# Optimization experiments

Measured on AMD Instinct MI355X. Metric: run time of the kernel, lower is better.

The kernel has to match this reference:

```python
import jax, jax.numpy as jnp
import numpy as np

B, L, K = 16, 512, 30          # proteins, residues per protein, kNN neighbors
N = B * L
H, FC = 32, 3                  # h_channels, frame_channels
C = H + FC                     # fused sphere channels (35)
HEADS, AC, VC = 8, 16, 8       # heads, alpha channels (H//2), value channels (H//4)
RBF_N, POS_N = 16, 16
EF = RBF_N + POS_N

# idealized backbone atom positions (N, CA, C) in the local residue frame
IDEAL_BB = np.array([[-0.525, 1.363, 0.0], [0.0, 0.0, 0.0], [1.526, 0.0, 0.0]], dtype=np.float32)
# cartesian (x,y,z) -> real-SH l=1 ordering (y,z,x)
P_SH = np.array([[0., 1., 0.], [0., 0., 1.], [1., 0., 0.]], dtype=np.float32)


def _knn_edges(trans):
    # per-chain brute-force kNN (chains are contiguous blocks of length L)
    X = trans.reshape(B, L, 3)
    d2 = jnp.sum((X[:, :, None, :] - X[:, None, :, :]) ** 2, axis=-1)  # [B,L,L]
    d2 = d2 + jnp.eye(L, dtype=d2.dtype) * 1e9                          # exclude self
    _, idx = jax.lax.top_k(-d2, K)                                      # [B,L,K]
    off = (jnp.arange(B) * L)[:, None, None]
    src = (idx + off).reshape(-1)              # neighbor (edge_index[0])
    tgt = jnp.repeat(jnp.arange(N), K)         # center   (edge_index[1])
    return src, tgt


def _edge_rot_mat(vec):
    # rotation aligning the edge vector with the y axis (eSCN init_edge_rot_mat style)
    nx = vec / (jnp.linalg.norm(vec, axis=-1, keepdims=True) + 1e-12)
    ref = jnp.where(jnp.abs(nx[:, :1]) < 0.9,
                    jnp.array([1., 0., 0.], dtype=vec.dtype),
                    jnp.array([0., 0., 1.], dtype=vec.dtype))
    nz = jnp.cross(nx, ref)
    nz = nz / (jnp.linalg.norm(nz, axis=-1, keepdims=True) + 1e-12)
    ny = jnp.cross(nx, nz)
    ny = ny / (jnp.linalg.norm(ny, axis=-1, keepdims=True) + 1e-12)
    return jnp.stack([nz, nx, ny], axis=-2)  # [E,3,3]


def _rbf(d, d_min=0.0, d_max=20.0, count=RBF_N):
    mu = jnp.linspace(d_min, d_max, count)
    sigma = (d_max - d_min) / count
    return jnp.exp(-(((d[:, None] - mu) / sigma) ** 2))


def _pos_emb(src, tgt, num=POS_N):
    d = (src - tgt).astype(jnp.float32)
    freq = jnp.exp(jnp.arange(0, num, 2, dtype=jnp.float32) * (-np.log(10000.0) / num))
    ang = d[:, None] * freq
    return jnp.concatenate([jnp.cos(ang), jnp.sin(ang)], axis=-1)


def _forward(rots, trans, node_emb, batch, x_mask, noising_mask,
             W_alpha, a_vec, W_v, W_o, W_g, W_2):
    src, tgt = _knn_edges(trans)
    vec = trans[src] - trans[tgt]
    dist = jnp.linalg.norm(vec, axis=-1)
    valid = jnp.isfinite(dist) & (dist > 1e-3)  # edge_select, applied as mask

    R = _edge_rot_mat(vec)
    P = jnp.asarray(P_SH)
    D1 = jnp.einsum('ij,ejk,lk->eil', P, R, P)  # l=1 Wigner in real-SH basis [E,3,3]

    edge_features = jnp.concatenate([_rbf(dist), _pos_emb(src, tgt)], axis=-1)  # [E,32]

    # fuse node features with backbone frame atoms and editability flag
    frame_atoms = jnp.einsum('nij,aj->nai', rots, jnp.asarray(IDEAL_BB))  # [N,3atoms,3xyz]
    editable = noising_mask & (~x_mask)
    emb = jnp.zeros((N, 4, C), dtype=node_emb.dtype)
    emb = emb.at[:, :, :H].set(node_emb)
    emb = emb.at[:, 1:4, H:].set(jnp.swapaxes(frame_atoms, -1, -2))
    emb = emb.at[:, 0, C - 1].set(editable.astype(node_emb.dtype))

    # gather + rotate source features into edge frames
    xs = emb[src]                                                   # [E,4,C]
    xs_rot = jnp.concatenate([xs[:, :1], jnp.einsum('eij,ejc->eic', D1, xs[:, 1:])], axis=1)

    # invariant attention logits (l=0 of rotated src, l=0 of tgt, edge feats)
    inv = jnp.concatenate([xs_rot[:, 0], emb[tgt, 0], edge_features], axis=-1)  # [E,102]
    hdn = jax.nn.silu(inv @ W_alpha).reshape(-1, HEADS, AC)
    logits = jax.nn.leaky_relu(jnp.einsum('ehk,hk->eh', hdn, a_vec), 0.2)
    logits = jnp.where(valid[:, None], logits, -1e9)

    # segment softmax over incoming edges of each target node
    mx = jax.lax.stop_gradient(jax.ops.segment_max(logits, tgt, num_segments=N))
    ex = jnp.exp(logits - mx[tgt]) * valid[:, None].astype(logits.dtype)
    den = jax.ops.segment_sum(ex, tgt, num_segments=N)
    alpha = ex / (den[tgt] + 1e-9)                                  # [E,HEADS]

    # equivariant values, attention-weighted, rotate back, scatter
    v = (xs_rot @ W_v).reshape(-1, 4, HEADS, VC)
    m = (v * alpha[:, None, :, None]).reshape(-1, 4, HEADS * VC)
    m = jnp.concatenate([m[:, :1], jnp.einsum('eji,ejc->eic', D1, m[:, 1:])], axis=1)  # D^T
    agg = jax.ops.segment_sum(m, tgt, num_segments=N)               # [N,4,64]

    y = agg @ W_o                                                    # [N,4,H]
    gate = jax.nn.silu(y[:, 0] @ W_g)                                # invariant gating FFN
    return (y * gate[:, None, :]) @ W_2                              # [N,4,H]


def setup_inputs():
    key = jax.random.key(0)
    ks = jax.random.split(key, 12)
    rots = jax.vmap(lambda m: jnp.linalg.qr(m)[0])(jax.random.normal(ks[0], (N, 3, 3)))
    trans = jax.random.normal(ks[1], (N, 3)) * 10.0
    node_emb = jax.random.normal(ks[2], (N, 4, H))
    batch = jnp.repeat(jnp.arange(B, dtype=jnp.int32), L)
    x_mask = jax.random.randint(ks[3], (N,), 0, 2).astype(bool)
    noising_mask = jax.random.randint(ks[4], (N,), 0, 2).astype(bool)
    s = lambda k, sh, fan: jax.random.normal(k, sh) / np.sqrt(fan)
    return dict(rots=rots, trans=trans, node_emb=node_emb, batch=batch,
                x_mask=x_mask, noising_mask=noising_mask,
                W_alpha=s(ks[5], (2 * C + EF, HEADS * AC), 2 * C + EF),
                a_vec=s(ks[6], (HEADS, AC), AC),
                W_v=s(ks[7], (C, HEADS * VC), C),
                W_o=s(ks[8], (HEADS * VC, H), HEADS * VC),
                W_g=s(ks[9], (H, H), H),
                W_2=s(ks[10], (H, H), H))


def reference(rots, trans, node_emb, batch, x_mask, noising_mask,
              W_alpha, a_vec, W_v, W_o, W_g, W_2):
    return _forward(rots, trans, node_emb, batch, x_mask, noising_mask,
                    W_alpha, a_vec, W_v, W_o, W_g, W_2)
```

## Files before the change

kernel.cpp:

```cpp
#include <hip/hip_runtime.h>
#include <cstdint>

#define B_ 16
#define L_ 512
#define N_ 8192
#define K_ 30
#define E_ (N_*K_)
#define H_ 32
#define C_ 35

typedef uint16_t u16;
typedef uint32_t u32;
typedef unsigned long long u64;
typedef float f2v __attribute__((ext_vector_type(2)));

static __device__ __forceinline__ f2v splat2(float x) { f2v v; v.x = x; v.y = x; return v; }

static __device__ __forceinline__ float ldf(const void* p, int i, int bf) {
    return bf ? __uint_as_float(((u32)((const u16*)p)[i]) << 16)
              : ((const float*)p)[i];
}
static __device__ __forceinline__ float bfu16(u16 x) {
    return __uint_as_float(((u32)x) << 16);
}
static __device__ __forceinline__ int ldmask(const void* p, int i, int mode) {
    if (mode == 0) return ((const unsigned char*)p)[i] != 0;
    if (mode == 2) return ((const u32*)p)[2*i] != 0;
    return ((const u32*)p)[i] != 0;
}
static __device__ __forceinline__ u16 f2bf(float f) {
    u32 x = __float_as_uint(f);
    u32 r = x + 0x7FFFu + ((x >> 16) & 1u);
    return (u16)(r >> 16);
}
static __device__ __forceinline__ float fsilu(float x) {
    return x * __builtin_amdgcn_rcpf(1.f + __expf(-x));
}
static __device__ __forceinline__ float RL(float x, int i) {
    return __uint_as_float((u32)__builtin_amdgcn_readlane((int)__float_as_uint(x), i));
}

static __device__ __forceinline__ int detect_bf(const void* tr, int lane) {
    const u16* p = (const u16*)tr;
    int cnt = 0;
    for (int i = lane; i < 256; i += 64) {
        u16 v = p[2 * i];
        int e = (v >> 7) & 0xFF;
        if ((e >= 100 && e <= 141) || (v & 0x7FFFu) == 0) cnt++;
    }
    #pragma unroll
    for (int d = 1; d < 64; d <<= 1) cnt += __shfl_xor(cnt, d, 64);
    return cnt >= 192;
}
static __device__ __forceinline__ int detect_mm(const void* xmv, int lane) {
    const u32* xm = (const u32*)xmv;
    int anyBig = 0, oddNZ = 0;
    for (int i = lane; i < 1024; i += 64) {
        u32 w = xm[i];
        if (w & ~1u) anyBig = 1;
        if ((i & 1) && w) oddNZ = 1;
    }
    #pragma unroll
    for (int d = 1; d < 64; d <<= 1) {
        anyBig |= __shfl_xor(anyBig, d, 64);
        oddNZ  |= __shfl_xor(oddNZ, d, 64);
    }
    return anyBig ? 0 : (oddNZ ? 1 : 2);
}

__constant__ float cBB[9] = {-0.525f, 1.363f, 0.f,  0.f, 0.f, 0.f,  1.526f, 0.f, 0.f};

#define DPP_UMIN(var, CTRL) \
    { u32 o_ = (u32)__builtin_amdgcn_update_dpp((int)(var), (int)(var), CTRL, 0xF, 0xF, false); \
      (var) = (o_ < (var)) ? o_ : (var); }
#define DPP_UMIN_ALL(var) \
    DPP_UMIN(var, 0x111) DPP_UMIN(var, 0x112) DPP_UMIN(var, 0x114) \
    DPP_UMIN(var, 0x118) DPP_UMIN(var, 0x142) DPP_UMIN(var, 0x143)

#define DPP_ADD8(part) \
    part += __uint_as_float((u32)__builtin_amdgcn_update_dpp( \
        (int)__float_as_uint(part), (int)__float_as_uint(part), 0xB1, 0xF, 0xF, false)); \
    part += __uint_as_float((u32)__builtin_amdgcn_update_dpp( \
        (int)__float_as_uint(part), (int)__float_as_uint(part), 0x4E, 0xF, 0xF, false)); \
    part += __uint_as_float((u32)__builtin_amdgcn_update_dpp( \
        (int)__float_as_uint(part), (int)__float_as_uint(part), 0x141, 0xF, 0xF, false));

__global__ __launch_bounds__(256) void knn_kernel(const void* __restrict__ trans,
                                                  const void* __restrict__ xm,
                                                  int* __restrict__ flag,
                                                  int* __restrict__ srcArr)
{
    __shared__ float sX[L_], sY[L_], sZ[L_];
    __shared__ int flagS[1];
    const int bid = blockIdx.x, tid = threadIdx.x;
    const int lane = tid & 63, wid = tid >> 6;

    if (wid == 0) {
        int bf = detect_bf(trans, lane);
        if (bid == 0) {
            int mm = detect_mm(xm, lane);
            if (lane == 0) { flag[0] = bf; flag[1] = mm; }
        }
        if (lane == 0) flagS[0] = bf;
    }
    __syncthreads();
    const int bf = flagS[0];
    const int t0 = bid * 4;
    const int base = (t0 >> 9) << 9;
    if (bf) {
        const u16* tp = (const u16*)trans;
        for (int i = tid; i < L_; i += 256) {
            sX[i] = bfu16(tp[(base + i) * 3 + 0]);
            sY[i] = bfu16(tp[(base + i) * 3 + 1]);
            sZ[i] = bfu16(tp[(base + i) * 3 + 2]);
        }
    } else {
        const float* tp = (const float*)trans;
        for (int i = tid; i < L_; i += 256) {
            sX[i] = tp[(base + i) * 3 + 0];
            sY[i] = tp[(base + i) * 3 + 1];
            sZ[i] = tp[(base + i) * 3 + 2];
        }
    }
    __syncthreads();

    const int t = t0 + wid;
    const int l = t & 511;
    const float tx = sX[l], ty = sY[l], tz = sZ[l];

    u32 d2b[8];
    #pragma unroll
    for (int i = 0; i < 8; ++i) {
        int j = lane + (i << 6);
        float dx = __fsub_rn(tx, sX[j]);
        float dy = __fsub_rn(ty, sY[j]);
        float dz = __fsub_rn(tz, sZ[j]);
        float d2 = __fadd_rn(__fadd_rn(__fmul_rn(dx, dx), __fmul_rn(dy, dy)), __fmul_rn(dz, dz));
        if (j == l) d2 = __fadd_rn(d2, 1e9f);
        d2b[i] = __float_as_uint(d2);
    }

    int myres = 0;
    for (int k = 0; k < K_; ++k) {
        u32 bb = d2b[0]; int bs = 0;
        #pragma unroll
        for (int i = 1; i < 8; ++i)
            if (d2b[i] < bb) { bb = d2b[i]; bs = i; }
        u32 m = bb;
        DPP_UMIN_ALL(m)
        u32 gbits = (u32)__builtin_amdgcn_readlane((int)m, 63);
        u64 mask = __ballot(bb == gbits);
        u32 gidx;
        if (__popcll(mask) == 1) {
            int wl = __ffsll((long long)mask) - 1;
            gidx = (u32)__builtin_amdgcn_readlane((int)((bs << 6) | lane), wl);
        } else {
            u32 cand = (bb == gbits) ? (u32)((bs << 6) | lane) : 0xFFFFFFFFu;
            DPP_UMIN_ALL(cand)
            gidx = (u32)__builtin_amdgcn_readlane((int)cand, 63);
        }
        if (lane == (u32)k) myres = (int)(gidx & 511u);
        if ((gidx & 63u) == (u32)lane) {
            int ws = (int)(gidx >> 6);
            #pragma unroll
            for (int i = 0; i < 8; ++i)
                if (ws == i) d2b[i] = 0xFFFFFFFFu;
        }
    }
    if (lane < K_) srcArr[t * K_ + lane] = base + myres;
}

__global__ __launch_bounds__(256) void prep_kernel(
    const void* __restrict__ rots, const void* __restrict__ node,
    const void* __restrict__ xm, const void* __restrict__ nm,
    const void* __restrict__ Wa, const void* __restrict__ av,
    const void* __restrict__ Wv, const void* __restrict__ Wo,
    const void* __restrict__ Wg, const void* __restrict__ W2,
    const int* __restrict__ flag,
    float* __restrict__ hsrc, float* __restrict__ htgt,
    float* __restrict__ ptab, float* __restrict__ V,
    float* __restrict__ c_wrb, float* __restrict__ c_av,
    float* __restrict__ c_Wo, float* __restrict__ c_Wg, float* __restrict__ c_W2)
{
    const int bid = blockIdx.x, tid = threadIdx.x;
    const int lane = tid & 63, wid = tid >> 6;
    const int bf = flag[0], mm = flag[1];

    if (bid < 2048) {
        const int n = bid * 4 + wid;

        float eA, eB, eC = 0.f;
        {
            int s = lane;
            int r = s / 35, c = s - r * 35;
            if (c < H_)      eA = ldf(node, n * 128 + r * 32 + c, bf);
            else if (r == 0) eA = (c == 34) ? ((ldmask(nm, n, mm) && !ldmask(xm, n, mm)) ? 1.f : 0.f) : 0.f;
            else {
                int i = r - 1, a = c - 32;
                eA = ldf(rots, n*9 + i*3 + 0, bf) * cBB[a*3 + 0]
                   + ldf(rots, n*9 + i*3 + 1, bf) * cBB[a*3 + 1]
                   + ldf(rots, n*9 + i*3 + 2, bf) * cBB[a*3 + 2];
            }
            s = lane + 64;
            r = s / 35; c = s - r * 35;
            if (c < H_)      eB = ldf(node, n * 128 + r * 32 + c, bf);
            else {
                int i = r - 1, a = c - 32;
                eB = ldf(rots, n*9 + i*3 + 0, bf) * cBB[a*3 + 0]
                   + ldf(rots, n*9 + i*3 + 1, bf) * cBB[a*3 + 1]
                   + ldf(rots, n*9 + i*3 + 2, bf) * cBB[a*3 + 2];
            }
            if (lane < 12) {
                s = lane + 128;
                r = s / 35; c = s - r * 35;
                if (c < H_)      eC = ldf(node, n * 128 + r * 32 + c, bf);
                else {
                    int i = r - 1, a = c - 32;
                    eC = ldf(rots, n*9 + i*3 + 0, bf) * cBB[a*3 + 0]
                       + ldf(rots, n*9 + i*3 + 1, bf) * cBB[a*3 + 1]
                       + ldf(rots, n*9 + i*3 + 2, bf) * cBB[a*3 + 2];
                }
            }
        }

        float a0 = 0.f, a1 = 0.f, b0 = 0.f, b1 = 0.f;
        float v0 = 0.f, v1 = 0.f, v2 = 0.f, v3 = 0.f;
        if (bf) {
            const u16* wa = (const u16*)Wa;
            const u16* wv = (const u16*)Wv;
            #pragma unroll
            for (int i = 0; i < 35; ++i) {
                float ei = RL(eA, i);
                a0 = fmaf(ei, bfu16(wa[i * 128 + lane]),        a0);
                a1 = fmaf(ei, bfu16(wa[i * 128 + lane + 64]),   a1);
                b0 = fmaf(ei, bfu16(wa[(35 + i) * 128 + lane]),      b0);
                b1 = fmaf(ei, bfu16(wa[(35 + i) * 128 + lane + 64]), b1);
            }
            #pragma unroll
            for (int cp = 0; cp < 35; ++cp) {
                float w = bfu16(wv[cp * 64 + lane]);
                float e1 = (35 + cp < 64) ? RL(eA, 35 + cp) : RL(eB, cp - 29);
                float e3 = (cp < 23) ? RL(eB, 41 + cp) : RL(eC, cp - 23);
                v0 = fmaf(RL(eA, cp), w, v0);
                v1 = fmaf(e1, w, v1);
                v2 = fmaf(RL(eB, cp + 6), w, v2);
                v3 = fmaf(e3, w, v3);
            }
        } else {
            const float* wa = (const float*)Wa;
            const float* wv = (const float*)Wv;
            #pragma unroll
            for (int i = 0; i < 35; ++i) {
                float ei = RL(eA, i);
                a0 = fmaf(ei, wa[i * 128 + lane],        a0);
                a1 = fmaf(ei, wa[i * 128 + lane + 64],   a1);
                b0 = fmaf(ei, wa[(35 + i) * 128 + lane],      b0);
                b1 = fmaf(ei, wa[(35 + i) * 128 + lane + 64], b1);
            }
            #pragma unroll
            for (int cp = 0; cp < 35; ++cp) {
                float w = wv[cp * 64 + lane];
                float e1 = (35 + cp < 64) ? RL(eA, 35 + cp) : RL(eB, cp - 29);
                float e3 = (cp < 23) ? RL(eB, 41 + cp) : RL(eC, cp - 23);
                v0 = fmaf(RL(eA, cp), w, v0);
                v1 = fmaf(e1, w, v1);
                v2 = fmaf(RL(eB, cp + 6), w, v2);
                v3 = fmaf(e3, w, v3);
            }
        }
        hsrc[(size_t)n * 128 + lane]      = a0;
        hsrc[(size_t)n * 128 + lane + 64] = a1;
        htgt[(size_t)n * 128 + lane]      = b0;
        htgt[(size_t)n * 128 + lane + 64] = b1;
        float* vp = V + (size_t)n * 256 + lane;
        vp[0] = v0; vp[64] = v1; vp[128] = v2; vp[192] = v3;

    } else if (bid < 2560) {
        const int d   = (bid - 2048) * 2 + (tid >> 7);
        const int col = tid & 127;
        float dd = (float)(d - 512);
        float acc = 0.f;
        if (bf) {
            const u16* wa = (const u16*)Wa;
            #pragma unroll
            for (int q = 0; q < 8; ++q) {
                float fr = expf((float)(2 * q) * (-0.5756462732485115f));
                float ang = dd * fr;
                acc = fmaf(cosf(ang), bfu16(wa[(86 + q) * 128 + col]), acc);
                acc = fmaf(sinf(ang), bfu16(wa[(94 + q) * 128 + col]), acc);
            }
        } else {
            const float* wa = (const float*)Wa;
            #pragma unroll
            for (int q = 0; q < 8; ++q) {
                float fr = expf((float)(2 * q) * (-0.5756462732485115f));
                float ang = dd * fr;
                acc = fmaf(cosf(ang), wa[(86 + q) * 128 + col], acc);
                acc = fmaf(sinf(ang), wa[(94 + q) * 128 + col], acc);
            }
        }
        ptab[(size_t)d * 128 + col] = acc;

    } else {
        int g0 = (bid - 2560) * 256 + tid;
        for (int i = g0; i < 6272; i += 2048) {
            if      (i < 2048) c_wrb[i]        = ldf(Wa, 70 * 128 + i, bf);
            else if (i < 2176) c_av[i - 2048]  = ldf(av, i - 2048, bf);
            else if (i < 4224) c_Wo[i - 2176]  = ldf(Wo, i - 2176, bf);
            else if (i < 5248) c_Wg[i - 4224]  = ldf(Wg, i - 4224, bf);
            else               c_W2[i - 5248]  = ldf(W2, i - 5248, bf);
        }
    }
}

__global__ __launch_bounds__(128) void logits_kernel(
    const void* __restrict__ trans, const int* __restrict__ srcArr,
    const float* __restrict__ hsrc, const float* __restrict__ htgt,
    const float* __restrict__ ptab,
    const float* __restrict__ c_wrb, const float* __restrict__ c_av,
    const int* __restrict__ flag, float* __restrict__ logitsw)
{
    __shared__ float rbfS[2][32][20];
    __shared__ int   srcS[2][32];
    __shared__ int   tgtS[2][32];
    __shared__ int   dS[2][32];
    __shared__ float lgS[2][256];
    const int tid = threadIdx.x, wid = tid >> 6, lane = tid & 63;
    const int bf = flag[0];

    const f2v* cw = (const f2v*)c_wrb;
    const f2v w0 = cw[0*64+lane],  w1 = cw[1*64+lane],  w2 = cw[2*64+lane],  w3 = cw[3*64+lane];
    const f2v w4 = cw[4*64+lane],  w5 = cw[5*64+lane],  w6 = cw[6*64+lane],  w7 = cw[7*64+lane];
    const f2v w8 = cw[8*64+lane],  w9 = cw[9*64+lane],  wA = cw[10*64+lane], wB = cw[11*64+lane];
    const f2v wC = cw[12*64+lane], wD = cw[13*64+lane], wE = cw[14*64+lane], wF = cw[15*64+lane];
    const f2v avv = ((const f2v*)c_av)[lane];

    const int e0 = (blockIdx.x * 2 + wid) * 32;

    {
        const int el  = lane & 31;
        const int e   = e0 + el;
        const int tgt = e / K_;
        int src = srcArr[e];
        src = (src < 0) ? 0 : ((src >= N_) ? (N_ - 1) : src);
        float vx = ldf(trans, src*3+0, bf) - ldf(trans, tgt*3+0, bf);
        float vy = ldf(trans, src*3+1, bf) - ldf(trans, tgt*3+1, bf);
        float vz = ldf(trans, src*3+2, bf) - ldf(trans, tgt*3+2, bf);
        float dist = sqrtf(vx*vx + vy*vy + vz*vz);
        bool valid = isfinite(dist) && (dist > 1e-3f);
        int d = src - tgt + 512;
        d = (d < 0) ? 0 : ((d > 1023) ? 1023 : d);
        if (lane < 32) {
            srcS[wid][el] = src;
            tgtS[wid][el] = tgt;
            dS[wid][el]   = d | (valid ? 0 : (1 << 16));
        }
        const int jb = (lane >> 5) * 8;
        #pragma unroll
        for (int j = 0; j < 8; ++j) {
            float tt = (dist - (float)(jb + j) * (20.f/15.f)) * 0.8f;
            rbfS[wid][el][jb + j] = __expf(-tt * tt);
        }
    }
    __syncthreads();

    const float* hsL = hsrc + (lane << 1);
    const float* htL = htgt + (lane << 1);
    const float* ptL = ptab + (lane << 1);
    #pragma unroll 2
    for (int q = 0; q < 32; ++q) {
        const int src = srcS[wid][q];
        const int tgt = tgtS[wid][q];
        const int dm  = dS[wid][q];
        const int d   = dm & 0xFFFF;
        const bool valid = (dm >> 16) == 0;

        f2v hs = *(const f2v*)(hsL + (src << 7));
        f2v ht = *(const f2v*)(htL + (tgt << 7));
        f2v pt = *(const f2v*)(ptL + (d << 7));
        f2v acc = (hs + ht) + pt;
        const float4* rp = (const float4*)(&rbfS[wid][q][0]);
        float4 ra = rp[0], rb = rp[1], rc = rp[2], rd = rp[3];
        acc = __builtin_elementwise_fma(splat2(ra.x), w0, acc);
        acc = __builtin_elementwise_fma(splat2(ra.y), w1, acc);
        acc = __builtin_elementwise_fma(splat2(ra.z), w2, acc);
        acc = __builtin_elementwise_fma(splat2(ra.w), w3, acc);
        acc = __builtin_elementwise_fma(splat2(rb.x), w4, acc);
        acc = __builtin_elementwise_fma(splat2(rb.y), w5, acc);
        acc = __builtin_elementwise_fma(splat2(rb.z), w6, acc);
        acc = __builtin_elementwise_fma(splat2(rb.w), w7, acc);
        acc = __builtin_elementwise_fma(splat2(rc.x), w8, acc);
        acc = __builtin_elementwise_fma(splat2(rc.y), w9, acc);
        acc = __builtin_elementwise_fma(splat2(rc.z), wA, acc);
        acc = __builtin_elementwise_fma(splat2(rc.w), wB, acc);
        acc = __builtin_elementwise_fma(splat2(rd.x), wC, acc);
        acc = __builtin_elementwise_fma(splat2(rd.y), wD, acc);
        acc = __builtin_elementwise_fma(splat2(rd.z), wE, acc);
        acc = __builtin_elementwise_fma(splat2(rd.w), wF, acc);
        float part = fsilu(acc.x) * avv.x + fsilu(acc.y) * avv.y;
        DPP_ADD8(part)
        float lg = (part >= 0.f) ? part : 0.2f * part;
        if (!valid) lg = -1e9f;
        lg = (fabsf(lg) < 1e30f) ? lg : -1e9f;
        if ((lane & 7) == 0) lgS[wid][q * 8 + (lane >> 3)] = lg;
    }
    __syncthreads();
    {
        float4* dst = (float4*)(logitsw + (size_t)e0 * 8);
        dst[lane] = ((const float4*)lgS[wid])[lane];
    }
}

__global__ __launch_bounds__(256) void agg_out_kernel(
    const float* __restrict__ V, const int* __restrict__ srcArr,
    const float* __restrict__ logitsw,
    const float* __restrict__ Wo, const float* __restrict__ Wg,
    const float* __restrict__ W2,
    const int* __restrict__ flag, void* __restrict__ outv)
{
    __shared__ float lgS[240];
    __shared__ float invS[8];
    __shared__ int   voffS[K_];
    __shared__ float aggS[256];
    __shared__ float ybuf[128];
    __shared__ float gbuf[32];
    const int bid = blockIdx.x, tid = threadIdx.x;
    const int t   = ((bid & 7) << 10) | (bid >> 3);
    const int bf = flag[0];

    if (tid < 240) lgS[tid] = logitsw[(size_t)t * 240 + tid];
    if (tid < K_) {
        int s = srcArr[t * K_ + tid];
        s = (s < 0) ? 0 : ((s >= N_) ? (N_ - 1) : s);
        voffS[tid] = s << 8;
    }
    __syncthreads();

    if (tid < 8) {
        float mx = -1e30f;
        #pragma unroll
        for (int k = 0; k < K_; ++k) mx = fmaxf(mx, lgS[k * 8 + tid]);
        float den = 0.f;
        #pragma unroll
        for (int k = 0; k < K_; ++k) {
            float l = lgS[k * 8 + tid];
            float e = (l > -1e8f) ? __expf(l - mx) : 0.f;
            lgS[k * 8 + tid] = e; den += e;
        }
        invS[tid] = 1.f / (den + 1e-9f);
    }
    __syncthreads();

    {
        const int h = (tid & 63) >> 3;
        float vv[K_];
        #pragma unroll
        for (int k = 0; k < K_; ++k) vv[k] = V[voffS[k] + tid];
        float acc = 0.f;
        #pragma unroll
        for (int k = 0; k < K_; ++k) acc = fmaf(lgS[k * 8 + h], vv[k], acc);
        aggS[tid] = acc * invS[h];
    }
    __syncthreads();

    if (tid < 128) {
        int rr = tid >> 5, o = tid & 31;
        float y = 0.f;
        #pragma unroll
        for (int c = 0; c < 64; ++c) y = fmaf(aggS[rr * 64 + c], Wo[c * 32 + o], y);
        ybuf[tid] = y;
    }
    __syncthreads();
    if (tid < 32) {
        float g = 0.f;
        #pragma unroll
        for (int o = 0; o < 32; ++o) g = fmaf(ybuf[o], Wg[o * 32 + tid], g);
        gbuf[tid] = fsilu(g);
    }
    __syncthreads();
    if (tid < 128) {
        int rr = tid >> 5, hh = tid & 31;
        float o = 0.f;
        #pragma unroll
        for (int g = 0; g < 32; ++g) o = fmaf(ybuf[rr * 32 + g] * gbuf[g], W2[g * 32 + hh], o);
        o = (fabsf(o) < 1e30f) ? o : 0.f;
        size_t idx = (size_t)t * 128 + tid;
        if (bf) ((u16*)outv)[idx] = f2bf(o);
        else    ((float*)outv)[idx] = o;
    }
}

extern "C" void kernel_launch(void* const* d_in, const int* in_sizes, int n_in,
                              void* d_out, int out_size, void* d_ws, size_t ws_size,
                              hipStream_t stream)
{
    const void* rots         = d_in[0];
    const void* trans        = d_in[1];
    const void* node_emb     = d_in[2];
    const void* x_mask       = d_in[4];
    const void* noising_mask = d_in[5];
    const void* Wa           = d_in[6];
    const void* avec         = d_in[7];
    const void* Wv           = d_in[8];
    const void* Wo           = d_in[9];
    const void* Wg           = d_in[10];
    const void* W2           = d_in[11];

    char* ws = (char*)d_ws;
    int*   flag    = (int*)  (ws + 0);
    int*   srcArr  = (int*)  (ws + 64);
    float* hsrc    = (float*)(ws + 983104);
    float* htgt    = (float*)(ws + 5177408);
    float* ptab    = (float*)(ws + 9371712);
    float* V       = (float*)(ws + 9896000);
    float* c_wrb   = (float*)(ws + 18284608);
    float* c_av    = (float*)(ws + 18292800);
    float* c_Wo    = (float*)(ws + 18293312);
    float* c_Wg    = (float*)(ws + 18301504);
    float* c_W2    = (float*)(ws + 18305600);
    float* logitsw = (float*)(ws + 18309696);

    hipLaunchKernelGGL(knn_kernel, dim3(N_/4), dim3(256), 0, stream,
                       trans, x_mask, flag, srcArr);
    hipLaunchKernelGGL(prep_kernel, dim3(2048 + 512 + 8), dim3(256), 0, stream,
                       rots, node_emb, x_mask, noising_mask,
                       Wa, avec, Wv, Wo, Wg, W2, flag,
                       hsrc, htgt, ptab, V,
                       c_wrb, c_av, c_Wo, c_Wg, c_W2);
    hipLaunchKernelGGL(logits_kernel, dim3(E_/64), dim3(128), 0, stream,
                       trans, srcArr, hsrc, htgt, ptab, c_wrb, c_av, flag, logitsw);
    hipLaunchKernelGGL(agg_out_kernel, dim3(N_), dim3(256), 0, stream,
                       V, srcArr, logitsw, c_Wo, c_Wg, c_W2, flag, d_out);
}
```

Baseline: 201.3 us.

## Merge kNN into prep kernel and fuse logits with aggregation per node

The kNN block range is folded into the prep kernel as an extra set of blocks, so those two stages run in one launch. The per-edge logits computation moves into the per-node aggregation kernel, which removes the logits workspace round trip and one more launch. The RBF FMAs now use inline-asm v_pk_fma_f32 with op_sel to broadcast pairs. Every block now runs the bf detection, and the node blocks run the mask detection too. The per-node kernel also computes 30 edges using only 4 waves, and that edge work is no longer spread across many blocks.

```diff
diff --git a/kernel.cpp b/kernel.cpp
--- a/kernel.cpp
+++ b/kernel.cpp
@@ -85,109 +85,109 @@
     part += __uint_as_float((u32)__builtin_amdgcn_update_dpp( \
         (int)__float_as_uint(part), (int)__float_as_uint(part), 0x141, 0xF, 0xF, false));
 
-__global__ __launch_bounds__(256) void knn_kernel(const void* __restrict__ trans,
-                                                  const void* __restrict__ xm,
-                                                  int* __restrict__ flag,
-                                                  int* __restrict__ srcArr)
-{
-    __shared__ float sX[L_], sY[L_], sZ[L_];
-    __shared__ int flagS[1];
-    const int bid = blockIdx.x, tid = threadIdx.x;
-    const int lane = tid & 63, wid = tid >> 6;
-
-    if (wid == 0) {
-        int bf = detect_bf(trans, lane);
-        if (bid == 0) {
-            int mm = detect_mm(xm, lane);
-            if (lane == 0) { flag[0] = bf; flag[1] = mm; }
-        }
-        if (lane == 0) flagS[0] = bf;
-    }
-    __syncthreads();
-    const int bf = flagS[0];
-    const int t0 = bid * 4;
-    const int base = (t0 >> 9) << 9;
-    if (bf) {
-        const u16* tp = (const u16*)trans;
-        for (int i = tid; i < L_; i += 256) {
-            sX[i] = bfu16(tp[(base + i) * 3 + 0]);
-            sY[i] = bfu16(tp[(base + i) * 3 + 1]);
-            sZ[i] = bfu16(tp[(base + i) * 3 + 2]);
-        }
-    } else {
-        const float* tp = (const float*)trans;
-        for (int i = tid; i < L_; i += 256) {
-            sX[i] = tp[(base + i) * 3 + 0];
-            sY[i] = tp[(base + i) * 3 + 1];
-            sZ[i] = tp[(base + i) * 3 + 2];
-        }
-    }
-    __syncthreads();
-
-    const int t = t0 + wid;
-    const int l = t & 511;
-    const float tx = sX[l], ty = sY[l], tz = sZ[l];
-
-    u32 d2b[8];
-    #pragma unroll
-    for (int i = 0; i < 8; ++i) {
-        int j = lane + (i << 6);
-        float dx = __fsub_rn(tx, sX[j]);
-        float dy = __fsub_rn(ty, sY[j]);
-        float dz = __fsub_rn(tz, sZ[j]);
-        float d2 = __fadd_rn(__fadd_rn(__fmul_rn(dx, dx), __fmul_rn(dy, dy)), __fmul_rn(dz, dz));
-        if (j == l) d2 = __fadd_rn(d2, 1e9f);
-        d2b[i] = __float_as_uint(d2);
-    }
-
-    int myres = 0;
-    for (int k = 0; k < K_; ++k) {
-        u32 bb = d2b[0]; int bs = 0;
-        #pragma unroll
-        for (int i = 1; i < 8; ++i)
-            if (d2b[i] < bb) { bb = d2b[i]; bs = i; }
-        u32 m = bb;
-        DPP_UMIN_ALL(m)
-        u32 gbits = (u32)__builtin_amdgcn_readlane((int)m, 63);
-        u64 mask = __ballot(bb == gbits);
-        u32 gidx;
-        if (__popcll(mask) == 1) {
-            int wl = __ffsll((long long)mask) - 1;
-            gidx = (u32)__builtin_amdgcn_readlane((int)((bs << 6) | lane), wl);
-        } else {
-            u32 cand = (bb == gbits) ? (u32)((bs << 6) | lane) : 0xFFFFFFFFu;
-            DPP_UMIN_ALL(cand)
-            gidx = (u32)__builtin_amdgcn_readlane((int)cand, 63);
-        }
-        if (lane == (u32)k) myres = (int)(gidx & 511u);
-        if ((gidx & 63u) == (u32)lane) {
-            int ws = (int)(gidx >> 6);
-            #pragma unroll
-            for (int i = 0; i < 8; ++i)
-                if (ws == i) d2b[i] = 0xFFFFFFFFu;
-        }
-    }
-    if (lane < K_) srcArr[t * K_ + lane] = base + myres;
-}
-
-__global__ __launch_bounds__(256) void prep_kernel(
-    const void* __restrict__ rots, const void* __restrict__ node,
+#define PKFMA_LO(acc, rr, w) \
+    asm("v_pk_fma_f32 %0, %1, %2, %0 op_sel:[0,0,0] op_sel_hi:[0,1,1]" \
+        : "+v"(acc) : "v"(rr), "v"(w))
+#define PKFMA_HI(acc, rr, w) \
+    asm("v_pk_fma_f32 %0, %1, %2, %0 op_sel:[1,0,0] op_sel_hi:[1,1,1]" \
+        : "+v"(acc) : "v"(rr), "v"(w))
+
+__global__ __launch_bounds__(256) void knn_prep_kernel(
+    const void* __restrict__ rots, const void* __restrict__ trans,
+    const void* __restrict__ node,
     const void* __restrict__ xm, const void* __restrict__ nm,
     const void* __restrict__ Wa, const void* __restrict__ av,
     const void* __restrict__ Wv, const void* __restrict__ Wo,
     const void* __restrict__ Wg, const void* __restrict__ W2,
-    const int* __restrict__ flag,
+    int* __restrict__ flag, int* __restrict__ srcArr,
     float* __restrict__ hsrc, float* __restrict__ htgt,
     float* __restrict__ ptab, float* __restrict__ V,
     float* __restrict__ c_wrb, float* __restrict__ c_av,
     float* __restrict__ c_Wo, float* __restrict__ c_Wg, float* __restrict__ c_W2)
 {
+    __shared__ float sX[L_], sY[L_], sZ[L_];
+    __shared__ int flagS[2];
     const int bid = blockIdx.x, tid = threadIdx.x;
     const int lane = tid & 63, wid = tid >> 6;
-    const int bf = flag[0], mm = flag[1];
+
+    if (wid == 0) {
+        int bfv = detect_bf(trans, lane);
+        int mmv = 0;
+        if (bid == 0 || (bid >= 2048 && bid < 4096)) mmv = detect_mm(xm, lane);
+        if (bid == 0 && lane == 0) { flag[0] = bfv; flag[1] = mmv; }
+        if (lane == 0) { flagS[0] = bfv; flagS[1] = mmv; }
+    }
+    __syncthreads();
+    const int bf = flagS[0];
 
     if (bid < 2048) {
-        const int n = bid * 4 + wid;
+        const int t0 = bid * 4;
+        const int base = (t0 >> 9) << 9;
+        if (bf) {
+            const u16* tp = (const u16*)trans;
+            for (int i = tid; i < L_; i += 256) {
+                sX[i] = bfu16(tp[(base + i) * 3 + 0]);
+                sY[i] = bfu16(tp[(base + i) * 3 + 1]);
+                sZ[i] = bfu16(tp[(base + i) * 3 + 2]);
+            }
+        } else {
+            const float* tp = (const float*)trans;
+            for (int i = tid; i < L_; i += 256) {
+                sX[i] = tp[(base + i) * 3 + 0];
+                sY[i] = tp[(base + i) * 3 + 1];
+                sZ[i] = tp[(base + i) * 3 + 2];
+            }
+        }
+        __syncthreads();
+
+        const int t = t0 + wid;
+        const int l = t & 511;
+        const float tx = sX[l], ty = sY[l], tz = sZ[l];
+
+        u32 d2b[8];
+        #pragma unroll
+        for (int i = 0; i < 8; ++i) {
+            int j = lane + (i << 6);
+            float dx = __fsub_rn(tx, sX[j]);
+            float dy = __fsub_rn(ty, sY[j]);
+            float dz = __fsub_rn(tz, sZ[j]);
+            float d2 = __fadd_rn(__fadd_rn(__fmul_rn(dx, dx), __fmul_rn(dy, dy)), __fmul_rn(dz, dz));
+            if (j == l) d2 = __fadd_rn(d2, 1e9f);
+            d2b[i] = __float_as_uint(d2);
+        }
+
+        int myres = 0;
+        for (int k = 0; k < K_; ++k) {
+            u32 bb = d2b[0]; int bs = 0;
+            #pragma unroll
+            for (int i = 1; i < 8; ++i)
+                if (d2b[i] < bb) { bb = d2b[i]; bs = i; }
+            u32 m = bb;
+            DPP_UMIN_ALL(m)
+            u32 gbits = (u32)__builtin_amdgcn_readlane((int)m, 63);
+            u64 mask = __ballot(bb == gbits);
+            u32 gidx;
+            if (__popcll(mask) == 1) {
+                int wl = __ffsll((long long)mask) - 1;
+                gidx = (u32)__builtin_amdgcn_readlane((int)((bs << 6) | lane), wl);
+            } else {
+                u32 cand = (bb == gbits) ? (u32)((bs << 6) | lane) : 0xFFFFFFFFu;
+                DPP_UMIN_ALL(cand)
+                gidx = (u32)__builtin_amdgcn_readlane((int)cand, 63);
+            }
+            if (lane == (u32)k) myres = (int)(gidx & 511u);
+            if ((gidx & 63u) == (u32)lane) {
+                int ws = (int)(gidx >> 6);
+                #pragma unroll
+                for (int i = 0; i < 8; ++i)
+                    if (ws == i) d2b[i] = 0xFFFFFFFFu;
+            }
+        }
+        if (lane < K_) srcArr[t * K_ + lane] = base + myres;
+
+    } else if (bid < 4096) {
+        const int mm = flagS[1];
+        const int n = (bid - 2048) * 4 + wid;
 
         float eA, eB, eC = 0.f;
         {
@@ -275,8 +275,8 @@
         float* vp = V + (size_t)n * 256 + lane;
         vp[0] = v0; vp[64] = v1; vp[128] = v2; vp[192] = v3;
 
-    } else if (bid < 2560) {
-        const int d   = (bid - 2048) * 2 + (tid >> 7);
+    } else if (bid < 4608) {
+        const int d   = (bid - 4096) * 2 + (tid >> 7);
         const int col = tid & 127;
         float dd = (float)(d - 512);
         float acc = 0.f;
@@ -302,7 +302,7 @@
         ptab[(size_t)d * 128 + col] = acc;
 
     } else {
-        int g0 = (bid - 2560) * 256 + tid;
+        int g0 = (bid - 4608) * 256 + tid;
         for (int i = g0; i < 6272; i += 2048) {
             if      (i < 2048) c_wrb[i]        = ldf(Wa, 70 * 128 + i, bf);
             else if (i < 2176) c_av[i - 2048]  = ldf(av, i - 2048, bf);
@@ -313,19 +313,29 @@
     }
 }
 
-__global__ __launch_bounds__(128) void logits_kernel(
+__global__ __launch_bounds__(256) void edge_agg_kernel(
     const void* __restrict__ trans, const int* __restrict__ srcArr,
     const float* __restrict__ hsrc, const float* __restrict__ htgt,
-    const float* __restrict__ ptab,
+    const float* __restrict__ ptab, const float* __restrict__ V,
     const float* __restrict__ c_wrb, const float* __restrict__ c_av,
-    const int* __restrict__ flag, float* __restrict__ logitsw)
+    const float* __restrict__ Wo, const float* __restrict__ Wg,
+    const float* __restrict__ W2,
+    const int* __restrict__ flag, void* __restrict__ outv)
 {
-    __shared__ float rbfS[2][32][20];
-    __shared__ int   srcS[2][32];
-    __shared__ int   tgtS[2][32];
-    __shared__ int   dS[2][32];
-    __shared__ float lgS[2][256];
-    const int tid = threadIdx.x, wid = tid >> 6, lane = tid & 63;
+    __shared__ __align__(16) float rbfS[K_][16];
+    __shared__ float lgS[240];
+    __shared__ int   hoffS[K_];
+    __shared__ int   pdS[K_];
+    __shared__ int   voffS[K_];
+    __shared__ int   valS[K_];
+    __shared__ float invS[8];
+    __shared__ float aggS[256];
+    __shared__ float ybuf[128];
+    __shared__ float gbuf[32];
+
+    const int bid = blockIdx.x, tid = threadIdx.x;
+    const int lane = tid & 63, wid = tid >> 6;
+    const int t = ((bid & 7) << 10) | (bid >> 3);
     const int bf = flag[0];
 
     const f2v* cw = (const f2v*)c_wrb;
@@ -334,105 +344,66 @@
     const f2v w8 = cw[8*64+lane],  w9 = cw[9*64+lane],  wA = cw[10*64+lane], wB = cw[11*64+lane];
     const f2v wC = cw[12*64+lane], wD = cw[13*64+lane], wE = cw[14*64+lane], wF = cw[15*64+lane];
     const f2v avv = ((const f2v*)c_av)[lane];
-
-    const int e0 = (blockIdx.x * 2 + wid) * 32;
-
-    {
-        const int el  = lane & 31;
-        const int e   = e0 + el;
-        const int tgt = e / K_;
-        int src = srcArr[e];
+    const f2v ht  = *(const f2v*)(htgt + ((size_t)t << 7) + (lane << 1));
+
+    if (tid < 240) {
+        const int k  = tid >> 3;
+        const int j2 = (tid & 7) << 1;
+        int src = srcArr[t * K_ + k];
         src = (src < 0) ? 0 : ((src >= N_) ? (N_ - 1) : src);
-        float vx = ldf(trans, src*3+0, bf) - ldf(trans, tgt*3+0, bf);
-        float vy = ldf(trans, src*3+1, bf) - ldf(trans, tgt*3+1, bf);
-        float vz = ldf(trans, src*3+2, bf) - ldf(trans, tgt*3+2, bf);
+        float vx = ldf(trans, src*3+0, bf) - ldf(trans, t*3+0, bf);
+        float vy = ldf(trans, src*3+1, bf) - ldf(trans, t*3+1, bf);
+        float vz = ldf(trans, src*3+2, bf) - ldf(trans, t*3+2, bf);
         float dist = sqrtf(vx*vx + vy*vy + vz*vz);
         bool valid = isfinite(dist) && (dist > 1e-3f);
-        int d = src - tgt + 512;
+        int d = src - t + 512;
         d = (d < 0) ? 0 : ((d > 1023) ? 1023 : d);
-        if (lane < 32) {
-            srcS[wid][el] = src;
-            tgtS[wid][el] = tgt;
-            dS[wid][el]   = d | (valid ? 0 : (1 << 16));
-        }
-        const int jb = (lane >> 5) * 8;
-        #pragma unroll
-        for (int j = 0; j < 8; ++j) {
-            float tt = (dist - (float)(jb + j) * (20.f/15.f)) * 0.8f;
-            rbfS[wid][el][jb + j] = __expf(-tt * tt);
-        }
-    }
-    __syncthreads();
-
-    const float* hsL = hsrc + (lane << 1);
-    const float* htL = htgt + (lane << 1);
-    const float* ptL = ptab + (lane << 1);
-    #pragma unroll 2
-    for (int q = 0; q < 32; ++q) {
-        const int src = srcS[wid][q];
-        const int tgt = tgtS[wid][q];
-        const int dm  = dS[wid][q];
-        const int d   = dm & 0xFFFF;
-        const bool valid = (dm >> 16) == 0;
-
-        f2v hs = *(const f2v*)(hsL + (src << 7));
-        f2v ht = *(const f2v*)(htL + (tgt << 7));
-        f2v pt = *(const f2v*)(ptL + (d << 7));
-        f2v acc = (hs + ht) + pt;
-        const float4* rp = (const float4*)(&rbfS[wid][q][0]);
-        float4 ra = rp[0], rb = rp[1], rc = rp[2], rd = rp[3];
-        acc = __builtin_elementwise_fma(splat2(ra.x), w0, acc);
-        acc = __builtin_elementwise_fma(splat2(ra.y), w1, acc);
-        acc = __builtin_elementwise_fma(splat2(ra.z), w2, acc);
-        acc = __builtin_elementwise_fma(splat2(ra.w), w3, acc);
-        acc = __builtin_elementwise_fma(splat2(rb.x), w4, acc);
-        acc = __builtin_elementwise_fma(splat2(rb.y), w5, acc);
-        acc = __builtin_elementwise_fma(splat2(rb.z), w6, acc);
-        acc = __builtin_elementwise_fma(splat2(rb.w), w7, acc);
-        acc = __builtin_elementwise_fma(splat2(rc.x), w8, acc);
-        acc = __builtin_elementwise_fma(splat2(rc.y), w9, acc);
-        acc = __builtin_elementwise_fma(splat2(rc.z), wA, acc);
-        acc = __builtin_elementwise_fma(splat2(rc.w), wB, acc);
-        acc = __builtin_elementwise_fma(splat2(rd.x), wC, acc);
-        acc = __builtin_elementwise_fma(splat2(rd.y), wD, acc);
-        acc = __builtin_elementwise_fma(splat2(rd.z), wE, acc);
-        acc = __builtin_elementwise_fma(splat2(rd.w), wF, acc);
-        float part = fsilu(acc.x) * avv.x + fsilu(acc.y) * avv.y;
-        DPP_ADD8(part)
-        float lg = (part >= 0.f) ? part : 0.2f * part;
-        if (!valid) lg = -1e9f;
-        lg = (fabsf(lg) < 1e30f) ? lg : -1e9f;
-        if ((lane & 7) == 0) lgS[wid][q * 8 + (lane >> 3)] = lg;
-    }
-    __syncthreads();
+        float ta = (dist - (float)j2       * (20.f/15.f)) * 0.8f;
+        float tb = (dist - (float)(j2 + 1) * (20.f/15.f)) * 0.8f;
+        rbfS[k][j2]     = __expf(-ta * ta);
+        rbfS[k][j2 + 1] = __expf(-tb * tb);
+        if ((tid & 7) == 0) {
+            hoffS[k] = src << 7;
+            pdS[k]   = d << 7;
+            voffS[k] = src << 8;
+            valS[k]  = valid ? 1 : 0;
+        }
+    }
+    __syncthreads();
+
     {
-        float4* dst = (float4*)(logitsw + (size_t)e0 * 8);
-        dst[lane] = ((const float4*)lgS[wid])[lane];
-    }
-}
-
-__global__ __launch_bounds__(256) void agg_out_kernel(
-    const float* __restrict__ V, const int* __restrict__ srcArr,
-    const float* __restrict__ logitsw,
-    const float* __restrict__ Wo, const float* __restrict__ Wg,
-    const float* __restrict__ W2,
-    const int* __restrict__ flag, void* __restrict__ outv)
-{
-    __shared__ float lgS[240];
-    __shared__ float invS[8];
-    __shared__ int   voffS[K_];
-    __shared__ float aggS[256];
-    __shared__ float ybuf[128];
-    __shared__ float gbuf[32];
-    const int bid = blockIdx.x, tid = threadIdx.x;
-    const int t   = ((bid & 7) << 10) | (bid >> 3);
-    const int bf = flag[0];
-
-    if (tid < 240) lgS[tid] = logitsw[(size_t)t * 240 + tid];
-    if (tid < K_) {
-        int s = srcArr[t * K_ + tid];
-        s = (s < 0) ? 0 : ((s >= N_) ? (N_ - 1) : s);
-        voffS[tid] = s << 8;
+        const int kBeg = wid * 8;
+        const int kEnd = (kBeg + 8 < K_) ? (kBeg + 8) : K_;
+        #pragma unroll 2
+        for (int k = kBeg; k < kEnd; ++k) {
+            f2v hs = *(const f2v*)(hsrc + hoffS[k] + (lane << 1));
+            f2v pt = *(const f2v*)(ptab + pdS[k]   + (lane << 1));
+            f2v acc = (hs + ht) + pt;
+            const float4* rp = (const float4*)(&rbfS[k][0]);
+            float4 ra = rp[0], rb = rp[1], rc = rp[2], rd = rp[3];
+            f2v r0; r0.x = ra.x; r0.y = ra.y;
+            f2v r1; r1.x = ra.z; r1.y = ra.w;
+            f2v r2; r2.x = rb.x; r2.y = rb.y;
+            f2v r3; r3.x = rb.z; r3.y = rb.w;
+            f2v r4; r4.x = rc.x; r4.y = rc.y;
+            f2v r5; r5.x = rc.z; r5.y = rc.w;
+            f2v r6; r6.x = rd.x; r6.y = rd.y;
+            f2v r7; r7.x = rd.z; r7.y = rd.w;
+            PKFMA_LO(acc, r0, w0); PKFMA_HI(acc, r0, w1);
+            PKFMA_LO(acc, r1, w2); PKFMA_HI(acc, r1, w3);
+            PKFMA_LO(acc, r2, w4); PKFMA_HI(acc, r2, w5);
+            PKFMA_LO(acc, r3, w6); PKFMA_HI(acc, r3, w7);
+            PKFMA_LO(acc, r4, w8); PKFMA_HI(acc, r4, w9);
+            PKFMA_LO(acc, r5, wA); PKFMA_HI(acc, r5, wB);
+            PKFMA_LO(acc, r6, wC); PKFMA_HI(acc, r6, wD);
+            PKFMA_LO(acc, r7, wE); PKFMA_HI(acc, r7, wF);
+            float part = fsilu(acc.x) * avv.x + fsilu(acc.y) * avv.y;
+            DPP_ADD8(part)
+            float lg = (part >= 0.f) ? part : 0.2f * part;
+            if (!valS[k]) lg = -1e9f;
+            lg = (fabsf(lg) < 1e30f) ? lg : -1e9f;
+            if ((lane & 7) == 0) lgS[k * 8 + (lane >> 3)] = lg;
+        }
     }
     __syncthreads();
 
@@ -518,17 +489,13 @@
     float* c_Wo    = (float*)(ws + 18293312);
     float* c_Wg    = (float*)(ws + 18301504);
     float* c_W2    = (float*)(ws + 18305600);
-    float* logitsw = (float*)(ws + 18309696);
-
-    hipLaunchKernelGGL(knn_kernel, dim3(N_/4), dim3(256), 0, stream,
-                       trans, x_mask, flag, srcArr);
-    hipLaunchKernelGGL(prep_kernel, dim3(2048 + 512 + 8), dim3(256), 0, stream,
-                       rots, node_emb, x_mask, noising_mask,
-                       Wa, avec, Wv, Wo, Wg, W2, flag,
-                       hsrc, htgt, ptab, V,
+
+    hipLaunchKernelGGL(knn_prep_kernel, dim3(2048 + 2048 + 512 + 8), dim3(256), 0, stream,
+                       rots, trans, node_emb, x_mask, noising_mask,
+                       Wa, avec, Wv, Wo, Wg, W2,
+                       flag, srcArr, hsrc, htgt, ptab, V,
                        c_wrb, c_av, c_Wo, c_Wg, c_W2);
-    hipLaunchKernelGGL(logits_kernel, dim3(E_/64), dim3(128), 0, stream,
-                       trans, srcArr, hsrc, htgt, ptab, c_wrb, c_av, flag, logitsw);
-    hipLaunchKernelGGL(agg_out_kernel, dim3(N_), dim3(256), 0, stream,
-                       V, srcArr, logitsw, c_Wo, c_Wg, c_W2, flag, d_out);
-}
+    hipLaunchKernelGGL(edge_agg_kernel, dim3(N_), dim3(256), 0, stream,
+                       trans, srcArr, hsrc, htgt, ptab, V,
+                       c_wrb, c_av, c_Wo, c_Wg, c_W2, flag, d_out);
+}
```

After: 209.0 us. 1.04x slower.
